# Optimization experiments

Hardware: AMD Instinct MI355X
Metric: run time of the kernel (lower is better)

Reference implementation:

```python
import jax, jax.numpy as jnp
import numpy as np

N = 50000      # nodes
DEG = 16       # incoming edges per node
E = N * DEG    # edges
F = 256        # nfeat
H = 8          # heads
DH = 32        # nhid // nheads
ALPHA = 0.2    # LeakyReLU negative slope


def setup_inputs() -> dict:
    key = jax.random.key(0)
    ks = jax.random.split(key, 6)
    h = jax.random.normal(ks[0], (N, F), jnp.float32)
    # xavier_uniform-like scale for W (gain 1.414)
    lim_w = 1.414 * np.sqrt(6.0 / (F + DH))
    W = jax.random.uniform(ks[1], (H, F, DH), jnp.float32, -lim_w, lim_w)
    bW = jnp.zeros((H, DH), jnp.float32)
    lim_a = 1.414 * np.sqrt(6.0 / (2 * DH + 1))
    a_src = jax.random.uniform(ks[2], (H, DH), jnp.float32, -lim_a, lim_a)
    a_dst = jax.random.uniform(ks[3], (H, DH), jnp.float32, -lim_a, lim_a)
    a_bias = jnp.zeros((H,), jnp.float32)
    src = jax.random.randint(ks[4], (E,), 0, N, dtype=jnp.int32)
    # every node gets exactly DEG incoming edges (ensures non-empty mailbox)
    dst = jnp.repeat(jnp.arange(N, dtype=jnp.int32), DEG)
    return {"h": h, "W": W, "bW": bW, "a_src": a_src, "a_dst": a_dst,
            "a_bias": a_bias, "src": src, "dst": dst}


def reference(h, W, bW, a_src, a_dst, a_bias, src, dst):
    # per-head projection: Wh[n,h,d]
    Wh = jnp.einsum('nf,hfd->nhd', h, W) + bW
    # decomposed attention linear: a([Wh_src, Wh_dst]) = s1[src] + s2[dst] + b
    s1 = jnp.einsum('nhd,hd->nh', Wh, a_src)   # [N,H]
    s2 = jnp.einsum('nhd,hd->nh', Wh, a_dst)   # [N,H]
    e = jax.nn.leaky_relu(s1[src] + s2[dst] + a_bias, ALPHA)  # [E,H]
    # segment softmax over incoming edges per destination node
    m = jax.ops.segment_max(e, dst, num_segments=N)           # [N,H]
    ex = jnp.exp(e - m[dst])
    denom = jax.ops.segment_sum(ex, dst, num_segments=N)      # [N,H]
    attn = ex / denom[dst]                                    # [E,H]
    # weighted scatter-sum aggregation of source features
    hp = jax.ops.segment_sum(attn[:, :, None] * Wh[src], dst, num_segments=N)  # [N,H,DH]
    # concat heads (matches torch.cat over head outputs)
    return hp.reshape(N, H * DH)
```

## Files before the change

kernel.cpp:

```cpp
#include <hip/hip_runtime.h>

#define NNODES 50000
#define FEAT 256
#define NH 8
#define DHEAD 32
#define DEG 16
#define CDIM 256

typedef __attribute__((ext_vector_type(4))) float floatx4;
typedef __attribute__((ext_vector_type(8))) short shortx8;
typedef __attribute__((ext_vector_type(8))) unsigned short ushortx8;

__device__ __forceinline__ unsigned short f2bf(float f) {
  union { float f; unsigned u; } v; v.f = f;
  unsigned r = v.u + 0x7fffu + ((v.u >> 16) & 1u);
  return (unsigned short)(r >> 16);
}
__device__ __forceinline__ float bf2f(unsigned short b) {
  union { unsigned u; float f; } v; v.u = ((unsigned)b) << 16;
  return v.f;
}

__global__ __launch_bounds__(256) void convert_wt(
    const float* __restrict__ W, unsigned short* __restrict__ Wt2) {
  int t = blockIdx.x * 256 + threadIdx.x;
#pragma unroll
  for (int p = 0; p < 4; ++p) {
    int idx = t * 4 + p;
    int jj = idx & 7;
    int l = (idx >> 3) & 63;
    int kt = (idx >> 9) & 7;
    int cgrp = idx >> 12;
    int c = cgrp * 16 + (l & 15);
    int f = kt * 32 + ((l >> 4) << 3) + jj;
    Wt2[idx] = f2bf(W[(size_t)(c >> 5) * (FEAT * DHEAD) + (size_t)f * DHEAD + (c & 31)]);
  }
}

__global__ __launch_bounds__(256) void gemm_fused(
    const float* __restrict__ h, const unsigned short* __restrict__ Wt2,
    const float* __restrict__ bW, const float* __restrict__ a_src,
    const float* __restrict__ a_dst, const float* __restrict__ a_bias,
    unsigned short* __restrict__ Whb, float* __restrict__ s1h,
    float* __restrict__ s2h) {
  __shared__ unsigned short As2[8 * 4 * 64 * 8];
  const int tid = threadIdx.x;
  const int w = tid >> 6, lane = tid & 63;
  const int mrow = lane & 15, quad = lane >> 4;
  const int row0 = blockIdx.x * 64;

  {
    int grow = row0 + w * 16 + mrow;
    if (grow > NNODES - 1) grow = NNODES - 1;
    const float* hp = h + (size_t)grow * FEAT + quad * 8;
#pragma unroll
    for (int kt = 0; kt < 8; ++kt) {
      float4 v0 = *(const float4*)(hp + kt * 32);
      float4 v1 = *(const float4*)(hp + kt * 32 + 4);
      shortx8 a8;
      a8[0] = (short)f2bf(v0.x); a8[1] = (short)f2bf(v0.y);
      a8[2] = (short)f2bf(v0.z); a8[3] = (short)f2bf(v0.w);
      a8[4] = (short)f2bf(v1.x); a8[5] = (short)f2bf(v1.y);
      a8[6] = (short)f2bf(v1.z); a8[7] = (short)f2bf(v1.w);
      *(shortx8*)&As2[((kt * 4 + w) * 64 + lane) * 8] = a8;
    }
  }
  __syncthreads();

  floatx4 acc[4][4] = {};
#pragma unroll
  for (int kt = 0; kt < 8; ++kt) {
    shortx8 af[4], bfr[4];
#pragma unroll
    for (int mi = 0; mi < 4; ++mi) {
      int cgrp = w * 4 + mi;
      bfr[mi] = *(const shortx8*)&Wt2[((size_t)(cgrp * 8 + kt) * 64 + lane) * 8];
    }
#pragma unroll
    for (int ni = 0; ni < 4; ++ni)
      af[ni] = *(const shortx8*)&As2[((kt * 4 + ni) * 64 + lane) * 8];
#pragma unroll
    for (int mi = 0; mi < 4; ++mi)
#pragma unroll
      for (int ni = 0; ni < 4; ++ni)
        acc[mi][ni] = __builtin_amdgcn_mfma_f32_16x16x32_bf16(
            bfr[mi], af[ni], acc[mi][ni], 0, 0, 0);
  }

  float4 bw4[4], as4[4], ad4[4];
#pragma unroll
  for (int mi = 0; mi < 4; ++mi) {
    int c0 = w * 64 + mi * 16 + quad * 4;
    bw4[mi] = *(const float4*)&bW[c0];
    as4[mi] = *(const float4*)&a_src[c0];
    ad4[mi] = *(const float4*)&a_dst[c0];
  }
  float ab0 = a_bias[w * 2], ab1 = a_bias[w * 2 + 1];

#pragma unroll
  for (int ni = 0; ni < 4; ++ni) {
    int n = row0 + ni * 16 + mrow;
    bool ok = n < NNODES;
    float p1h0 = 0.f, p1h1 = 0.f, p2h0 = 0.f, p2h1 = 0.f;
#pragma unroll
    for (int mi = 0; mi < 4; ++mi) {
      int c0 = w * 64 + mi * 16 + quad * 4;
      float v0 = acc[mi][ni][0] + bw4[mi].x;
      float v1 = acc[mi][ni][1] + bw4[mi].y;
      float v2 = acc[mi][ni][2] + bw4[mi].z;
      float v3 = acc[mi][ni][3] + bw4[mi].w;
      ushort4 u;
      u.x = f2bf(v0); u.y = f2bf(v1); u.z = f2bf(v2); u.w = f2bf(v3);
      if (ok)
        *(ushort4*)&Whb[(size_t)(c0 >> 5) * ((size_t)NNODES * 32) +
                        (size_t)n * 32 + (c0 & 31)] = u;
      float d1 = v0 * as4[mi].x + v1 * as4[mi].y + v2 * as4[mi].z + v3 * as4[mi].w;
      float d2 = v0 * ad4[mi].x + v1 * ad4[mi].y + v2 * ad4[mi].z + v3 * ad4[mi].w;
      if (mi < 2) { p1h0 += d1; p2h0 += d2; }
      else        { p1h1 += d1; p2h1 += d2; }
    }
    p1h0 += __shfl_xor(p1h0, 16); p1h0 += __shfl_xor(p1h0, 32);
    p1h1 += __shfl_xor(p1h1, 16); p1h1 += __shfl_xor(p1h1, 32);
    p2h0 += __shfl_xor(p2h0, 16); p2h0 += __shfl_xor(p2h0, 32);
    p2h1 += __shfl_xor(p2h1, 16); p2h1 += __shfl_xor(p2h1, 32);
    if (quad == 0 && ok) {
      s1h[(size_t)(w * 2) * NNODES + n] = p1h0;
      s1h[(size_t)(w * 2 + 1) * NNODES + n] = p1h1;
      s2h[(size_t)(w * 2) * NNODES + n] = p2h0 + ab0;
      s2h[(size_t)(w * 2 + 1) * NNODES + n] = p2h1 + ab1;
    }
  }
}

__global__ __launch_bounds__(256) void aggregate(
    const unsigned short* __restrict__ Whb, const float* __restrict__ s1h,
    const float* __restrict__ s2h, const int* __restrict__ src,
    float* __restrict__ out) {
  const int lane = threadIdx.x & 63;
  const int wv = threadIdx.x >> 6;
  const int b = blockIdx.x;
  const int hh = b & 7;
  const int c = lane & 3;
  int n = (b >> 3) * 64 + wv * 16 + (lane >> 2);
  const bool valid = n < NNODES;
  if (!valid) n = NNODES - 1;

  const int4* srow = (const int4*)&src[(size_t)n * DEG];
  int4 s0 = srow[0], s1 = srow[1], s2 = srow[2], s3 = srow[3];

  const unsigned short* Wh = Whb + (size_t)hh * ((size_t)NNODES * 32) + c * 8;
  ushortx8 v0  = *(const ushortx8*)&Wh[(size_t)s0.x * 32];
  ushortx8 v1  = *(const ushortx8*)&Wh[(size_t)s0.y * 32];
  ushortx8 v2  = *(const ushortx8*)&Wh[(size_t)s0.z * 32];
  ushortx8 v3  = *(const ushortx8*)&Wh[(size_t)s0.w * 32];
  ushortx8 v4  = *(const ushortx8*)&Wh[(size_t)s1.x * 32];
  ushortx8 v5  = *(const ushortx8*)&Wh[(size_t)s1.y * 32];
  ushortx8 v6  = *(const ushortx8*)&Wh[(size_t)s1.z * 32];
  ushortx8 v7  = *(const ushortx8*)&Wh[(size_t)s1.w * 32];
  ushortx8 v8  = *(const ushortx8*)&Wh[(size_t)s2.x * 32];
  ushortx8 v9  = *(const ushortx8*)&Wh[(size_t)s2.y * 32];
  ushortx8 v10 = *(const ushortx8*)&Wh[(size_t)s2.z * 32];
  ushortx8 v11 = *(const ushortx8*)&Wh[(size_t)s2.w * 32];
  ushortx8 v12 = *(const ushortx8*)&Wh[(size_t)s3.x * 32];
  ushortx8 v13 = *(const ushortx8*)&Wh[(size_t)s3.y * 32];
  ushortx8 v14 = *(const ushortx8*)&Wh[(size_t)s3.z * 32];
  ushortx8 v15 = *(const ushortx8*)&Wh[(size_t)s3.w * 32];

  int4 se = c == 0 ? s0 : (c == 1 ? s1 : (c == 2 ? s2 : s3));
  const float* s1p = s1h + (size_t)hh * NNODES;
  float a0 = s1p[se.x], a1 = s1p[se.y], a2 = s1p[se.z], a3 = s1p[se.w];
  float s2n = s2h[(size_t)hh * NNODES + n];

  float t0 = a0 + s2n, t1 = a1 + s2n, t2 = a2 + s2n, t3 = a3 + s2n;
  t0 = t0 > 0.f ? t0 : 0.2f * t0;
  t1 = t1 > 0.f ? t1 : 0.2f * t1;
  t2 = t2 > 0.f ? t2 : 0.2f * t2;
  t3 = t3 > 0.f ? t3 : 0.2f * t3;
  float e0 = __expf(t0), e1 = __expf(t1), e2 = __expf(t2), e3 = __expf(t3);
  float sum = (e0 + e1) + (e2 + e3);
  sum += __shfl_xor(sum, 1);
  sum += __shfl_xor(sum, 2);
  float inv = 1.f / sum;

  float acc0 = 0.f, acc1 = 0.f, acc2 = 0.f, acc3 = 0.f;
  float acc4 = 0.f, acc5 = 0.f, acc6 = 0.f, acc7 = 0.f;
#define STEP(K, EV, VV)                                            \
  {                                                                \
    float wk = __shfl(EV, (lane & 60) | (K >> 2)) * inv;           \
    acc0 += wk * bf2f(VV[0]); acc1 += wk * bf2f(VV[1]);            \
    acc2 += wk * bf2f(VV[2]); acc3 += wk * bf2f(VV[3]);            \
    acc4 += wk * bf2f(VV[4]); acc5 += wk * bf2f(VV[5]);            \
    acc6 += wk * bf2f(VV[6]); acc7 += wk * bf2f(VV[7]);            \
  }
  STEP(0, e0, v0)   STEP(1, e1, v1)   STEP(2, e2, v2)   STEP(3, e3, v3)
  STEP(4, e0, v4)   STEP(5, e1, v5)   STEP(6, e2, v6)   STEP(7, e3, v7)
  STEP(8, e0, v8)   STEP(9, e1, v9)   STEP(10, e2, v10) STEP(11, e3, v11)
  STEP(12, e0, v12) STEP(13, e1, v13) STEP(14, e2, v14) STEP(15, e3, v15)
#undef STEP

  if (valid) {
    float* op = &out[(size_t)n * CDIM + hh * 32 + c * 8];
    floatx4 o0, o1;
    o0.x = acc0; o0.y = acc1; o0.z = acc2; o0.w = acc3;
    o1.x = acc4; o1.y = acc5; o1.z = acc6; o1.w = acc7;
    __builtin_nontemporal_store(o0, (floatx4*)op);
    __builtin_nontemporal_store(o1, (floatx4*)(op + 4));
  }
}

extern "C" void kernel_launch(void* const* d_in, const int* in_sizes, int n_in,
                              void* d_out, int out_size, void* d_ws, size_t ws_size,
                              hipStream_t stream) {
  const float* h = (const float*)d_in[0];
  const float* W = (const float*)d_in[1];
  const float* bW = (const float*)d_in[2];
  const float* a_src = (const float*)d_in[3];
  const float* a_dst = (const float*)d_in[4];
  const float* a_bias = (const float*)d_in[5];
  const int* src = (const int*)d_in[6];
  float* out = (float*)d_out;

  unsigned short* Whb = (unsigned short*)d_ws;
  unsigned short* Wt2 = Whb + (size_t)NNODES * CDIM;
  float* s1h = (float*)(Wt2 + CDIM * FEAT);
  float* s2h = s1h + (size_t)NH * NNODES;

  convert_wt<<<64, 256, 0, stream>>>(W, Wt2);
  gemm_fused<<<(NNODES + 63) / 64, 256, 0, stream>>>(h, Wt2, bW, a_src, a_dst,
                                                     a_bias, Whb, s1h, s2h);
  aggregate<<<782 * 8, 256, 0, stream>>>(Whb, s1h, s2h, src, out);
}
```

Measured before the change: 178.0 us.

## Make aggregate kernel persistent with prefetch of next node group's edge indices

Turns the aggregation kernel into a persistent grid of 768 blocks (96 per head) that loop over node groups with a stride. The next group's src indices are prefetched while the current group's gathers and softmax are computed, and src loads become nontemporal. A launch bound of 3 is added to cap registers. The aim is to hide the dependent index-then-gather latency and cut block launch overhead, at the cost of fewer resident waves and more register pressure.

```diff
diff --git a/kernel.cpp b/kernel.cpp
--- a/kernel.cpp
+++ b/kernel.cpp
@@ -10,6 +10,7 @@
 typedef __attribute__((ext_vector_type(4))) float floatx4;
 typedef __attribute__((ext_vector_type(8))) short shortx8;
 typedef __attribute__((ext_vector_type(8))) unsigned short ushortx8;
+typedef __attribute__((ext_vector_type(4))) int intx4;
 
 __device__ __forceinline__ unsigned short f2bf(float f) {
   union { float f; unsigned u; } v; v.f = f;
@@ -132,7 +133,7 @@
   }
 }
 
-__global__ __launch_bounds__(256) void aggregate(
+__global__ __launch_bounds__(256, 3) void aggregate(
     const unsigned short* __restrict__ Whb, const float* __restrict__ s1h,
     const float* __restrict__ s2h, const int* __restrict__ src,
     float* __restrict__ out) {
@@ -141,70 +142,99 @@
   const int b = blockIdx.x;
   const int hh = b & 7;
   const int c = lane & 3;
-  int n = (b >> 3) * 64 + wv * 16 + (lane >> 2);
-  const bool valid = n < NNODES;
-  if (!valid) n = NNODES - 1;
-
-  const int4* srow = (const int4*)&src[(size_t)n * DEG];
-  int4 s0 = srow[0], s1 = srow[1], s2 = srow[2], s3 = srow[3];
-
+  const int nl = lane >> 2;
   const unsigned short* Wh = Whb + (size_t)hh * ((size_t)NNODES * 32) + c * 8;
-  ushortx8 v0  = *(const ushortx8*)&Wh[(size_t)s0.x * 32];
-  ushortx8 v1  = *(const ushortx8*)&Wh[(size_t)s0.y * 32];
-  ushortx8 v2  = *(const ushortx8*)&Wh[(size_t)s0.z * 32];
-  ushortx8 v3  = *(const ushortx8*)&Wh[(size_t)s0.w * 32];
-  ushortx8 v4  = *(const ushortx8*)&Wh[(size_t)s1.x * 32];
-  ushortx8 v5  = *(const ushortx8*)&Wh[(size_t)s1.y * 32];
-  ushortx8 v6  = *(const ushortx8*)&Wh[(size_t)s1.z * 32];
-  ushortx8 v7  = *(const ushortx8*)&Wh[(size_t)s1.w * 32];
-  ushortx8 v8  = *(const ushortx8*)&Wh[(size_t)s2.x * 32];
-  ushortx8 v9  = *(const ushortx8*)&Wh[(size_t)s2.y * 32];
-  ushortx8 v10 = *(const ushortx8*)&Wh[(size_t)s2.z * 32];
-  ushortx8 v11 = *(const ushortx8*)&Wh[(size_t)s2.w * 32];
-  ushortx8 v12 = *(const ushortx8*)&Wh[(size_t)s3.x * 32];
-  ushortx8 v13 = *(const ushortx8*)&Wh[(size_t)s3.y * 32];
-  ushortx8 v14 = *(const ushortx8*)&Wh[(size_t)s3.z * 32];
-  ushortx8 v15 = *(const ushortx8*)&Wh[(size_t)s3.w * 32];
-
-  int4 se = c == 0 ? s0 : (c == 1 ? s1 : (c == 2 ? s2 : s3));
   const float* s1p = s1h + (size_t)hh * NNODES;
-  float a0 = s1p[se.x], a1 = s1p[se.y], a2 = s1p[se.z], a3 = s1p[se.w];
-  float s2n = s2h[(size_t)hh * NNODES + n];
-
-  float t0 = a0 + s2n, t1 = a1 + s2n, t2 = a2 + s2n, t3 = a3 + s2n;
-  t0 = t0 > 0.f ? t0 : 0.2f * t0;
-  t1 = t1 > 0.f ? t1 : 0.2f * t1;
-  t2 = t2 > 0.f ? t2 : 0.2f * t2;
-  t3 = t3 > 0.f ? t3 : 0.2f * t3;
-  float e0 = __expf(t0), e1 = __expf(t1), e2 = __expf(t2), e3 = __expf(t3);
-  float sum = (e0 + e1) + (e2 + e3);
-  sum += __shfl_xor(sum, 1);
-  sum += __shfl_xor(sum, 2);
-  float inv = 1.f / sum;
-
-  float acc0 = 0.f, acc1 = 0.f, acc2 = 0.f, acc3 = 0.f;
-  float acc4 = 0.f, acc5 = 0.f, acc6 = 0.f, acc7 = 0.f;
+  const float* s2p = s2h + (size_t)hh * NNODES;
+  const int NG = (NNODES + 63) / 64;
+  const int BPH = 96;
+
+  int g = b >> 3;
+  int n = g * 64 + wv * 16 + nl;
+  bool vcur = n < NNODES;
+  int ncl = vcur ? n : NNODES - 1;
+  const intx4* sp0 = (const intx4*)&src[(size_t)ncl * DEG];
+  intx4 p0 = __builtin_nontemporal_load(sp0);
+  intx4 p1 = __builtin_nontemporal_load(sp0 + 1);
+  intx4 p2 = __builtin_nontemporal_load(sp0 + 2);
+  intx4 p3 = __builtin_nontemporal_load(sp0 + 3);
+
+  while (true) {
+    intx4 se = c == 0 ? p0 : (c == 1 ? p1 : (c == 2 ? p2 : p3));
+    float a0 = s1p[se.x], a1 = s1p[se.y], a2 = s1p[se.z], a3 = s1p[se.w];
+    float s2n = s2p[ncl];
+
+    ushortx8 v0  = *(const ushortx8*)&Wh[(size_t)p0.x * 32];
+    ushortx8 v1  = *(const ushortx8*)&Wh[(size_t)p0.y * 32];
+    ushortx8 v2  = *(const ushortx8*)&Wh[(size_t)p0.z * 32];
+    ushortx8 v3  = *(const ushortx8*)&Wh[(size_t)p0.w * 32];
+    ushortx8 v4  = *(const ushortx8*)&Wh[(size_t)p1.x * 32];
+    ushortx8 v5  = *(const ushortx8*)&Wh[(size_t)p1.y * 32];
+    ushortx8 v6  = *(const ushortx8*)&Wh[(size_t)p1.z * 32];
+    ushortx8 v7  = *(const ushortx8*)&Wh[(size_t)p1.w * 32];
+    ushortx8 v8  = *(const ushortx8*)&Wh[(size_t)p2.x * 32];
+    ushortx8 v9  = *(const ushortx8*)&Wh[(size_t)p2.y * 32];
+    ushortx8 v10 = *(const ushortx8*)&Wh[(size_t)p2.z * 32];
+    ushortx8 v11 = *(const ushortx8*)&Wh[(size_t)p2.w * 32];
+    ushortx8 v12 = *(const ushortx8*)&Wh[(size_t)p3.x * 32];
+    ushortx8 v13 = *(const ushortx8*)&Wh[(size_t)p3.y * 32];
+    ushortx8 v14 = *(const ushortx8*)&Wh[(size_t)p3.z * 32];
+    ushortx8 v15 = *(const ushortx8*)&Wh[(size_t)p3.w * 32];
+
+    int gn = g + BPH;
+    int nn = gn * 64 + wv * 16 + nl;
+    bool vnx = nn < NNODES;
+    int nncl = vnx ? nn : NNODES - 1;
+    intx4 q0 = {0, 0, 0, 0}, q1 = {0, 0, 0, 0};
+    intx4 q2 = {0, 0, 0, 0}, q3 = {0, 0, 0, 0};
+    if (gn < NG) {
+      const intx4* sq = (const intx4*)&src[(size_t)nncl * DEG];
+      q0 = __builtin_nontemporal_load(sq);
+      q1 = __builtin_nontemporal_load(sq + 1);
+      q2 = __builtin_nontemporal_load(sq + 2);
+      q3 = __builtin_nontemporal_load(sq + 3);
+    }
+
+    float t0 = a0 + s2n, t1 = a1 + s2n, t2 = a2 + s2n, t3 = a3 + s2n;
+    t0 = t0 > 0.f ? t0 : 0.2f * t0;
+    t1 = t1 > 0.f ? t1 : 0.2f * t1;
+    t2 = t2 > 0.f ? t2 : 0.2f * t2;
+    t3 = t3 > 0.f ? t3 : 0.2f * t3;
+    float e0 = __expf(t0), e1 = __expf(t1), e2 = __expf(t2), e3 = __expf(t3);
+    float sum = (e0 + e1) + (e2 + e3);
+    sum += __shfl_xor(sum, 1);
+    sum += __shfl_xor(sum, 2);
+    float inv = 1.f / sum;
+
+    float acc0 = 0.f, acc1 = 0.f, acc2 = 0.f, acc3 = 0.f;
+    float acc4 = 0.f, acc5 = 0.f, acc6 = 0.f, acc7 = 0.f;
 #define STEP(K, EV, VV)                                            \
-  {                                                                \
-    float wk = __shfl(EV, (lane & 60) | (K >> 2)) * inv;           \
-    acc0 += wk * bf2f(VV[0]); acc1 += wk * bf2f(VV[1]);            \
-    acc2 += wk * bf2f(VV[2]); acc3 += wk * bf2f(VV[3]);            \
-    acc4 += wk * bf2f(VV[4]); acc5 += wk * bf2f(VV[5]);            \
-    acc6 += wk * bf2f(VV[6]); acc7 += wk * bf2f(VV[7]);            \
-  }
-  STEP(0, e0, v0)   STEP(1, e1, v1)   STEP(2, e2, v2)   STEP(3, e3, v3)
-  STEP(4, e0, v4)   STEP(5, e1, v5)   STEP(6, e2, v6)   STEP(7, e3, v7)
-  STEP(8, e0, v8)   STEP(9, e1, v9)   STEP(10, e2, v10) STEP(11, e3, v11)
-  STEP(12, e0, v12) STEP(13, e1, v13) STEP(14, e2, v14) STEP(15, e3, v15)
+    {                                                              \
+      float wk = __shfl(EV, (lane & 60) | (K >> 2)) * inv;         \
+      acc0 += wk * bf2f(VV[0]); acc1 += wk * bf2f(VV[1]);          \
+      acc2 += wk * bf2f(VV[2]); acc3 += wk * bf2f(VV[3]);          \
+      acc4 += wk * bf2f(VV[4]); acc5 += wk * bf2f(VV[5]);          \
+      acc6 += wk * bf2f(VV[6]); acc7 += wk * bf2f(VV[7]);          \
+    }
+    STEP(0, e0, v0)   STEP(1, e1, v1)   STEP(2, e2, v2)   STEP(3, e3, v3)
+    STEP(4, e0, v4)   STEP(5, e1, v5)   STEP(6, e2, v6)   STEP(7, e3, v7)
+    STEP(8, e0, v8)   STEP(9, e1, v9)   STEP(10, e2, v10) STEP(11, e3, v11)
+    STEP(12, e0, v12) STEP(13, e1, v13) STEP(14, e2, v14) STEP(15, e3, v15)
 #undef STEP
 
-  if (valid) {
-    float* op = &out[(size_t)n * CDIM + hh * 32 + c * 8];
-    floatx4 o0, o1;
-    o0.x = acc0; o0.y = acc1; o0.z = acc2; o0.w = acc3;
-    o1.x = acc4; o1.y = acc5; o1.z = acc6; o1.w = acc7;
-    __builtin_nontemporal_store(o0, (floatx4*)op);
-    __builtin_nontemporal_store(o1, (floatx4*)(op + 4));
+    if (vcur) {
+      float* op = &out[(size_t)n * CDIM + hh * 32 + c * 8];
+      floatx4 o0, o1;
+      o0.x = acc0; o0.y = acc1; o0.z = acc2; o0.w = acc3;
+      o1.x = acc4; o1.y = acc5; o1.z = acc6; o1.w = acc7;
+      __builtin_nontemporal_store(o0, (floatx4*)op);
+      __builtin_nontemporal_store(o1, (floatx4*)(op + 4));
+    }
+
+    g = gn;
+    if (g >= NG) break;
+    n = nn; ncl = nncl; vcur = vnx;
+    p0 = q0; p1 = q1; p2 = q2; p3 = q3;
   }
 }
 
@@ -228,5 +258,5 @@
   convert_wt<<<64, 256, 0, stream>>>(W, Wt2);
   gemm_fused<<<(NNODES + 63) / 64, 256, 0, stream>>>(h, Wt2, bW, a_src, a_dst,
                                                      a_bias, Whb, s1h, s2h);
-  aggregate<<<782 * 8, 256, 0, stream>>>(Whb, s1h, s2h, src, out);
-}
+  aggregate<<<8 * 96, 256, 0, stream>>>(Whb, s1h, s2h, src, out);
+}
```

Result: slower. 194.6 us (+9.3%).

## Split attention softmax into separate scores kernel with fp16 weights and node-major scores

Applied to the files above, without the earlier changes.

Changes the s1/s2 score layout from head-major to node-major so all 8 heads of a node come from one 32-byte read. Adds a scores kernel that computes leaky-relu, exp and the per-node softmax once for all heads and writes normalized fp16 attention weights. The aggregate kernel then reads precomputed weights instead of doing random s1 gathers and exps per head-block. The trade-off is an extra launch plus writing and reading an E×H fp16 buffer (about 12.8 MB), and fp16 weights lose some precision.

```diff
diff --git a/kernel.cpp b/kernel.cpp
--- a/kernel.cpp
+++ b/kernel.cpp
@@ -10,6 +10,8 @@
 typedef __attribute__((ext_vector_type(4))) float floatx4;
 typedef __attribute__((ext_vector_type(8))) short shortx8;
 typedef __attribute__((ext_vector_type(8))) unsigned short ushortx8;
+typedef __attribute__((ext_vector_type(4))) int intx4;
+typedef __attribute__((ext_vector_type(4))) _Float16 halfx4;
 
 __device__ __forceinline__ unsigned short f2bf(float f) {
   union { float f; unsigned u; } v; v.f = f;
@@ -41,8 +43,8 @@
     const float* __restrict__ h, const unsigned short* __restrict__ Wt2,
     const float* __restrict__ bW, const float* __restrict__ a_src,
     const float* __restrict__ a_dst, const float* __restrict__ a_bias,
-    unsigned short* __restrict__ Whb, float* __restrict__ s1h,
-    float* __restrict__ s2h) {
+    unsigned short* __restrict__ Whb, float* __restrict__ s1g,
+    float* __restrict__ s2g) {
   __shared__ unsigned short As2[8 * 4 * 64 * 8];
   const int tid = threadIdx.x;
   const int w = tid >> 6, lane = tid & 63;
@@ -124,18 +126,56 @@
     p2h0 += __shfl_xor(p2h0, 16); p2h0 += __shfl_xor(p2h0, 32);
     p2h1 += __shfl_xor(p2h1, 16); p2h1 += __shfl_xor(p2h1, 32);
     if (quad == 0 && ok) {
-      s1h[(size_t)(w * 2) * NNODES + n] = p1h0;
-      s1h[(size_t)(w * 2 + 1) * NNODES + n] = p1h1;
-      s2h[(size_t)(w * 2) * NNODES + n] = p2h0 + ab0;
-      s2h[(size_t)(w * 2 + 1) * NNODES + n] = p2h1 + ab1;
-    }
+      float2 s1v; s1v.x = p1h0; s1v.y = p1h1;
+      float2 s2v; s2v.x = p2h0 + ab0; s2v.y = p2h1 + ab1;
+      *(float2*)&s1g[(size_t)n * NH + w * 2] = s1v;
+      *(float2*)&s2g[(size_t)n * NH + w * 2] = s2v;
+    }
+  }
+}
+
+__global__ __launch_bounds__(256) void scores(
+    const float* __restrict__ s1g, const float* __restrict__ s2g,
+    const int* __restrict__ src, _Float16* __restrict__ attw) {
+  const int lane = threadIdx.x & 63;
+  const int wv = threadIdx.x >> 6;
+  const int nl = lane >> 4, e = lane & 15;
+  const int n = blockIdx.x * 16 + wv * 4 + nl;
+
+  int s = src[(size_t)n * DEG + e];
+  float4 f1a = *(const float4*)&s1g[(size_t)s * NH];
+  float4 f1b = *(const float4*)&s1g[(size_t)s * NH + 4];
+  float4 f2a = *(const float4*)&s2g[(size_t)n * NH];
+  float4 f2b = *(const float4*)&s2g[(size_t)n * NH + 4];
+
+  float sc[8];
+  sc[0] = f1a.x + f2a.x; sc[1] = f1a.y + f2a.y;
+  sc[2] = f1a.z + f2a.z; sc[3] = f1a.w + f2a.w;
+  sc[4] = f1b.x + f2b.x; sc[5] = f1b.y + f2b.y;
+  sc[6] = f1b.z + f2b.z; sc[7] = f1b.w + f2b.w;
+  float ex[8], sm[8];
+#pragma unroll
+  for (int hh = 0; hh < 8; ++hh) {
+    float t = sc[hh];
+    t = t > 0.f ? t : 0.2f * t;
+    ex[hh] = __expf(t);
+    float su = ex[hh];
+    su += __shfl_xor(su, 1);
+    su += __shfl_xor(su, 2);
+    su += __shfl_xor(su, 4);
+    su += __shfl_xor(su, 8);
+    sm[hh] = su;
+  }
+#pragma unroll
+  for (int hh = 0; hh < 8; ++hh) {
+    float w = ex[hh] * (1.f / sm[hh]);
+    attw[(size_t)hh * (NNODES * DEG) + (size_t)n * DEG + e] = (_Float16)w;
   }
 }
 
 __global__ __launch_bounds__(256) void aggregate(
-    const unsigned short* __restrict__ Whb, const float* __restrict__ s1h,
-    const float* __restrict__ s2h, const int* __restrict__ src,
-    float* __restrict__ out) {
+    const unsigned short* __restrict__ Whb, const _Float16* __restrict__ attw,
+    const int* __restrict__ src, float* __restrict__ out) {
   const int lane = threadIdx.x & 63;
   const int wv = threadIdx.x >> 6;
   const int b = blockIdx.x;
@@ -145,58 +185,54 @@
   const bool valid = n < NNODES;
   if (!valid) n = NNODES - 1;
 
-  const int4* srow = (const int4*)&src[(size_t)n * DEG];
-  int4 s0 = srow[0], s1 = srow[1], s2 = srow[2], s3 = srow[3];
+  halfx4 w4 = *(const halfx4*)&attw[(size_t)hh * (NNODES * DEG) +
+                                    (size_t)n * DEG + c * 4];
+  float wA = (float)w4[0], wB = (float)w4[1];
+  float wC = (float)w4[2], wD = (float)w4[3];
+
+  const intx4* srow = (const intx4*)&src[(size_t)n * DEG];
+  intx4 p0 = srow[0], p1 = srow[1], p2 = srow[2], p3 = srow[3];
 
   const unsigned short* Wh = Whb + (size_t)hh * ((size_t)NNODES * 32) + c * 8;
-  ushortx8 v0  = *(const ushortx8*)&Wh[(size_t)s0.x * 32];
-  ushortx8 v1  = *(const ushortx8*)&Wh[(size_t)s0.y * 32];
-  ushortx8 v2  = *(const ushortx8*)&Wh[(size_t)s0.z * 32];
-  ushortx8 v3  = *(const ushortx8*)&Wh[(size_t)s0.w * 32];
-  ushortx8 v4  = *(const ushortx8*)&Wh[(size_t)s1.x * 32];
-  ushortx8 v5  = *(const ushortx8*)&Wh[(size_t)s1.y * 32];
-  ushortx8 v6  = *(const ushortx8*)&Wh[(size_t)s1.z * 32];
-  ushortx8 v7  = *(const ushortx8*)&Wh[(size_t)s1.w * 32];
-  ushortx8 v8  = *(const ushortx8*)&Wh[(size_t)s2.x * 32];
-  ushortx8 v9  = *(const ushortx8*)&Wh[(size_t)s2.y * 32];
-  ushortx8 v10 = *(const ushortx8*)&Wh[(size_t)s2.z * 32];
-  ushortx8 v11 = *(const ushortx8*)&Wh[(size_t)s2.w * 32];
-  ushortx8 v12 = *(const ushortx8*)&Wh[(size_t)s3.x * 32];
-  ushortx8 v13 = *(const ushortx8*)&Wh[(size_t)s3.y * 32];
-  ushortx8 v14 = *(const ushortx8*)&Wh[(size_t)s3.z * 32];
-  ushortx8 v15 = *(const ushortx8*)&Wh[(size_t)s3.w * 32];
-
-  int4 se = c == 0 ? s0 : (c == 1 ? s1 : (c == 2 ? s2 : s3));
-  const float* s1p = s1h + (size_t)hh * NNODES;
-  float a0 = s1p[se.x], a1 = s1p[se.y], a2 = s1p[se.z], a3 = s1p[se.w];
-  float s2n = s2h[(size_t)hh * NNODES + n];
-
-  float t0 = a0 + s2n, t1 = a1 + s2n, t2 = a2 + s2n, t3 = a3 + s2n;
-  t0 = t0 > 0.f ? t0 : 0.2f * t0;
-  t1 = t1 > 0.f ? t1 : 0.2f * t1;
-  t2 = t2 > 0.f ? t2 : 0.2f * t2;
-  t3 = t3 > 0.f ? t3 : 0.2f * t3;
-  float e0 = __expf(t0), e1 = __expf(t1), e2 = __expf(t2), e3 = __expf(t3);
-  float sum = (e0 + e1) + (e2 + e3);
-  sum += __shfl_xor(sum, 1);
-  sum += __shfl_xor(sum, 2);
-  float inv = 1.f / sum;
+  ushortx8 v0  = *(const ushortx8*)&Wh[(size_t)p0.x * 32];
+  ushortx8 v1  = *(const ushortx8*)&Wh[(size_t)p0.y * 32];
+  ushortx8 v2  = *(const ushortx8*)&Wh[(size_t)p0.z * 32];
+  ushortx8 v3  = *(const ushortx8*)&Wh[(size_t)p0.w * 32];
+  ushortx8 v4  = *(const ushortx8*)&Wh[(size_t)p1.x * 32];
+  ushortx8 v5  = *(const ushortx8*)&Wh[(size_t)p1.y * 32];
+  ushortx8 v6  = *(const ushortx8*)&Wh[(size_t)p1.z * 32];
+  ushortx8 v7  = *(const ushortx8*)&Wh[(size_t)p1.w * 32];
+  ushortx8 v8  = *(const ushortx8*)&Wh[(size_t)p2.x * 32];
+  ushortx8 v9  = *(const ushortx8*)&Wh[(size_t)p2.y * 32];
+  ushortx8 v10 = *(const ushortx8*)&Wh[(size_t)p2.z * 32];
+  ushortx8 v11 = *(const ushortx8*)&Wh[(size_t)p2.w * 32];
+  ushortx8 v12 = *(const ushortx8*)&Wh[(size_t)p3.x * 32];
+  ushortx8 v13 = *(const ushortx8*)&Wh[(size_t)p3.y * 32];
+  ushortx8 v14 = *(const ushortx8*)&Wh[(size_t)p3.z * 32];
+  ushortx8 v15 = *(const ushortx8*)&Wh[(size_t)p3.w * 32];
 
   float acc0 = 0.f, acc1 = 0.f, acc2 = 0.f, acc3 = 0.f;
   float acc4 = 0.f, acc5 = 0.f, acc6 = 0.f, acc7 = 0.f;
-#define STEP(K, EV, VV)                                            \
+#define ACC8(WK, VV)                                               \
   {                                                                \
-    float wk = __shfl(EV, (lane & 60) | (K >> 2)) * inv;           \
+    float wk = (WK);                                               \
     acc0 += wk * bf2f(VV[0]); acc1 += wk * bf2f(VV[1]);            \
     acc2 += wk * bf2f(VV[2]); acc3 += wk * bf2f(VV[3]);            \
     acc4 += wk * bf2f(VV[4]); acc5 += wk * bf2f(VV[5]);            \
     acc6 += wk * bf2f(VV[6]); acc7 += wk * bf2f(VV[7]);            \
   }
-  STEP(0, e0, v0)   STEP(1, e1, v1)   STEP(2, e2, v2)   STEP(3, e3, v3)
-  STEP(4, e0, v4)   STEP(5, e1, v5)   STEP(6, e2, v6)   STEP(7, e3, v7)
-  STEP(8, e0, v8)   STEP(9, e1, v9)   STEP(10, e2, v10) STEP(11, e3, v11)
-  STEP(12, e0, v12) STEP(13, e1, v13) STEP(14, e2, v14) STEP(15, e3, v15)
-#undef STEP
+#define STEP4(CC, VA, VB, VC, VD)                                  \
+  {                                                                \
+    int sl = (lane & 60) | CC;                                     \
+    ACC8(__shfl(wA, sl), VA); ACC8(__shfl(wB, sl), VB);            \
+    ACC8(__shfl(wC, sl), VC); ACC8(__shfl(wD, sl), VD);            \
+  }
+  STEP4(0, v0, v1, v2, v3)
+  STEP4(1, v4, v5, v6, v7)
+  STEP4(2, v8, v9, v10, v11)
+  STEP4(3, v12, v13, v14, v15)
+#undef STEP4
+#undef ACC8
 
   if (valid) {
     float* op = &out[(size_t)n * CDIM + hh * 32 + c * 8];
@@ -222,11 +258,13 @@
 
   unsigned short* Whb = (unsigned short*)d_ws;
   unsigned short* Wt2 = Whb + (size_t)NNODES * CDIM;
-  float* s1h = (float*)(Wt2 + CDIM * FEAT);
-  float* s2h = s1h + (size_t)NH * NNODES;
+  float* s1g = (float*)(Wt2 + CDIM * FEAT);
+  float* s2g = s1g + (size_t)NNODES * NH;
+  _Float16* attw = (_Float16*)(s2g + (size_t)NNODES * NH);
 
   convert_wt<<<64, 256, 0, stream>>>(W, Wt2);
   gemm_fused<<<(NNODES + 63) / 64, 256, 0, stream>>>(h, Wt2, bW, a_src, a_dst,
-                                                     a_bias, Whb, s1h, s2h);
-  aggregate<<<782 * 8, 256, 0, stream>>>(Whb, s1h, s2h, src, out);
-}
+                                                     a_bias, Whb, s1g, s2g);
+  scores<<<NNODES / 16, 256, 0, stream>>>(s1g, s2g, src, attw);
+  aggregate<<<782 * 8, 256, 0, stream>>>(Whb, attw, src, out);
+}
```

Result: faster. 171.8 us (-3.5%).
